# Optimization experiments

Hardware: AMD Instinct MI355X
Metric: run time of the kernel (lower is better)

## Reference

```python
import jax, jax.numpy as jnp
import numpy as np

N = 100000
INPLANES = 256
WIDTH = 104          # floor(256 * 26 / 64)
SCALE = 4
NUMS = SCALE - 1     # 3 branch convs
K = 27               # 3^3 kernel offsets for 3D kernel_size=3
EPS = 1e-5


def setup_inputs() -> dict:
    key = jax.random.key(0)
    ks = jax.random.split(key, 12)
    x_feat = jax.random.normal(ks[0], (N, INPLANES), dtype=jnp.float32)
    # neighbor map: index N means "no neighbor" (padded zero row)
    nbr_idx = jax.random.randint(ks[1], (N, K), 0, N + 1)
    ws = WIDTH * SCALE
    W1 = jax.random.normal(ks[2], (INPLANES, ws), dtype=jnp.float32) * (1.0 / np.sqrt(INPLANES))
    g1 = jnp.ones((ws,), jnp.float32)
    b1 = jnp.zeros((ws,), jnp.float32)
    Wc = jax.random.normal(ks[3], (NUMS, K, WIDTH, WIDTH), dtype=jnp.float32) * (1.0 / np.sqrt(K * WIDTH))
    gc = jnp.ones((NUMS, WIDTH), jnp.float32)
    bc = jnp.zeros((NUMS, WIDTH), jnp.float32)
    W3 = jax.random.normal(ks[4], (ws, INPLANES), dtype=jnp.float32) * (1.0 / np.sqrt(ws))
    g3 = jnp.ones((INPLANES,), jnp.float32)
    b3 = jnp.zeros((INPLANES,), jnp.float32)
    return {"x_feat": x_feat, "nbr_idx": nbr_idx, "W1": W1, "g1": g1, "b1": b1,
            "Wc": Wc, "gc": gc, "bc": bc, "W3": W3, "g3": g3, "b3": b3}


def _bn(x, g, b):
    # training-mode batch norm over the point dimension
    m = jnp.mean(x, axis=0)
    v = jnp.var(x, axis=0)
    return (x - m) * jax.lax.rsqrt(v + EPS) * g + b


def _sparse_conv(feat, nbr_idx, Wk):
    # gather-GEMM-scatter sparse conv: out[n] = sum_k feat[nbr[n,k]] @ Wk[k]
    # index == N hits the appended zero row (missing neighbor)
    fp = jnp.concatenate([feat, jnp.zeros((1, feat.shape[1]), feat.dtype)], axis=0)
    out = jnp.zeros((feat.shape[0], Wk.shape[2]), feat.dtype)
    for k in range(Wk.shape[0]):  # fixed small set of 27 kernel offsets
        out = out + fp[nbr_idx[:, k]] @ Wk[k]
    return out


def reference(x_feat, nbr_idx, W1, g1, b1, Wc, gc, bc, W3, g3, b3):
    out = jax.nn.relu(_bn(x_feat @ W1, g1, b1))          # [N, width*scale]
    spx = [out[:, i * WIDTH:(i + 1) * WIDTH] for i in range(SCALE)]
    parts = []
    sp = None
    for i in range(NUMS):
        # stype='normal', same coord map -> features_at_coordinates is identity
        sp_in = spx[i] if i == 0 else sp + spx[i]
        sp = jax.nn.relu(_bn(_sparse_conv(sp_in, nbr_idx, Wc[i]), gc[i], bc[i]))
        parts.append(sp)
    parts.append(spx[SCALE - 1])                          # scale != 1, normal
    cat = jnp.concatenate(parts, axis=1)                  # [N, width*scale]
    out = _bn(cat @ W3, g3, b3) + x_feat                  # residual (no downsample)
    return jax.nn.relu(out)
```

## Files before the change

### kernel.cpp

```cpp
#include <hip/hip_runtime.h>

#define NPTS 100000
#define INC 256
#define WID 104
#define WSC 416
#define KOFF 27
#define EPSV 1e-5f

typedef unsigned short u16;
typedef float f32x4 __attribute__((ext_vector_type(4)));
typedef short s16x8 __attribute__((ext_vector_type(8)));

__device__ __forceinline__ u16 f2bf(float f) {
  unsigned u = __builtin_bit_cast(unsigned, f);
  u += 0x7FFFu + ((u >> 16) & 1u);
  return (u16)(u >> 16);
}
__device__ __forceinline__ float bf2f(u16 h) {
  unsigned u = ((unsigned)h) << 16;
  return __builtin_bit_cast(float, u);
}
__device__ __forceinline__ void mfma16(f32x4& d, s16x8 a, s16x8 b) {
  asm("v_mfma_f32_16x16x32_bf16 %0, %1, %2, %0" : "+v"(d) : "v"(a), "v"(b));
}
__device__ __forceinline__ void rawbar() {
  __builtin_amdgcn_s_barrier();
  __builtin_amdgcn_sched_barrier(0);
}

#define ST1_OFF 0
#define STC0_OFF 7488
#define STC1_OFF 9360
#define STC2_OFF 11232
#define ST3_OFF 13104
#define ST_TOTAL 17712

__global__ __launch_bounds__(256) void k_prep_w1w3(const float* __restrict__ w1,
    const float* __restrict__ w3, u16* __restrict__ w1t, u16* __restrict__ w3t) {
  int i = blockIdx.x * 256 + threadIdx.x;
  if (i < 416 * 256) {
    int n = i >> 8, k = i & 255;
    w1t[i] = f2bf(w1[(size_t)k * WSC + n]);
  } else if (i < 2 * 416 * 256) {
    int o = i - 416 * 256;
    int n = o / WSC, k = o - n * WSC;
    w3t[o] = f2bf(w3[(size_t)k * INC + n]);
  }
}

__global__ __launch_bounds__(256) void k_prep_wc(const float* __restrict__ wc,
                                                 u16* __restrict__ wct) {
  __shared__ float w[WID * WID];
  int b = blockIdx.x, t = threadIdx.x;
  const float* s = wc + (size_t)b * WID * WID;
  for (int i = t; i < WID * WID; i += 256) w[i] = s[i];
  __syncthreads();
  u16* d = wct + (size_t)b * 112 * WID;
  for (int o = t; o < 112 * WID; o += 256) {
    int n = o / WID, kin = o - n * WID;
    d[o] = f2bf((n < WID) ? w[kin * WID + n] : 0.f);
  }
}

__global__ void k_init(float* __restrict__ st, u16* __restrict__ spxrow) {
  int i = blockIdx.x * 256 + threadIdx.x;
  if (i < ST_TOTAL) st[i] = 0.f;
  else if (i < ST_TOTAL + 104) spxrow[i - ST_TOTAL] = 0;
}

__global__ __launch_bounds__(256) void k_xbf(const float* __restrict__ x,
                                             u16* __restrict__ xb) {
  const int total = NPTS * INC / 8;
  for (int i = blockIdx.x * 256 + threadIdx.x; i < total; i += gridDim.x * 256) {
    const f32x4* s = (const f32x4*)(x + (size_t)i * 8);
    f32x4 v0 = s[0], v1 = s[1];
    s16x8 h;
#pragma unroll
    for (int j = 0; j < 4; ++j) { h[j] = (short)f2bf(v0[j]); h[4 + j] = (short)f2bf(v1[j]); }
    *(s16x8*)(xb + (size_t)i * 8) = h;
  }
}

__global__ __launch_bounds__(256) void k_gemm1(const u16* __restrict__ xb,
    const u16* __restrict__ w1t, u16* __restrict__ y1, float* __restrict__ stats) {
  __shared__ char Al[128 * 128];
  __shared__ char Bl[112 * 128];
  const int t = threadIdx.x, rowbase = blockIdx.x * 128, cb = blockIdx.y;
  const int lane = t & 63, wv = t >> 6, lr = lane & 15, lg = lane >> 4;
  const f32x4 fz = {0.f, 0.f, 0.f, 0.f};
  const s16x8 hz = {0, 0, 0, 0, 0, 0, 0, 0};
  f32x4 acc[2][7];
#pragma unroll
  for (int i = 0; i < 2; ++i)
#pragma unroll
    for (int j = 0; j < 7; ++j) acc[i][j] = fz;
  s16x8 pa[4], pb[4];

  auto issue = [&](int st) {
#pragma unroll
    for (int it = 0; it < 4; ++it) {
      int task = t + it * 256, r = task >> 3, c = task & 7, gr = rowbase + r;
      pa[it] = hz;
      if (gr < NPTS) pa[it] = *(const s16x8*)(xb + (size_t)gr * INC + st * 64 + c * 8);
      pb[it] = hz;
      if (task < 832)
        pb[it] = *(const s16x8*)(w1t + (size_t)(cb * WID + r) * INC + st * 64 + c * 8);
    }
  };
  auto writeT = [&]() {
#pragma unroll
    for (int it = 0; it < 4; ++it) {
      int task = t + it * 256, r = task >> 3, c = task & 7;
      *(s16x8*)(Al + ((r * 128 + c * 16) ^ ((r & 7) << 4))) = pa[it];
      if (task < 896) *(s16x8*)(Bl + ((r * 128 + c * 16) ^ ((r & 7) << 4))) = pb[it];
    }
  };
  auto compute = [&]() {
#pragma unroll
    for (int kc = 0; kc < 2; ++kc) {
      int co = kc * 64 + lg * 16;
      s16x8 a[2], b[7];
#pragma unroll
      for (int mt = 0; mt < 2; ++mt) {
        int r = wv * 32 + mt * 16 + lr;
        a[mt] = *(const s16x8*)(Al + ((r * 128 + co) ^ ((r & 7) << 4)));
      }
#pragma unroll
      for (int ct = 0; ct < 7; ++ct) {
        int r = ct * 16 + lr;
        b[ct] = *(const s16x8*)(Bl + ((r * 128 + co) ^ ((r & 7) << 4)));
      }
#pragma unroll
      for (int mt = 0; mt < 2; ++mt)
#pragma unroll
        for (int ct = 0; ct < 7; ++ct) mfma16(acc[mt][ct], a[mt], b[ct]);
    }
  };

  issue(0);
  for (int st = 0; st < 4; ++st) {
    writeT();
    __syncthreads();
    if (st < 3) issue(st + 1);
    compute();
    if (st < 3) rawbar();
  }
  __syncthreads();
  float* S = (float*)Al;
#pragma unroll
  for (int ct = 0; ct < 7; ++ct) {
    float s = 0.f, q = 0.f;
#pragma unroll
    for (int mt = 0; mt < 2; ++mt)
#pragma unroll
      for (int j = 0; j < 4; ++j) { float v = acc[mt][ct][j]; s += v; q += v * v; }
    s += __shfl_xor(s, 16); s += __shfl_xor(s, 32);
    q += __shfl_xor(q, 16); q += __shfl_xor(q, 32);
    if (lane < 16) {
      S[wv * 224 + ct * 16 + lane] = s;
      S[wv * 224 + 112 + ct * 16 + lane] = q;
    }
  }
  __syncthreads();
  if (t < 224) {
    float v = S[t] + S[224 + t] + S[448 + t] + S[672 + t];
    int cl = (t < 112) ? t : t - 112;
    if (cl < WID) {
      float* base = stats + (blockIdx.x & 7) * 832;
      atomicAdd(base + ((t < 112) ? 0 : WSC) + cb * WID + cl, v);
    }
  }
  __syncthreads();
#pragma unroll
  for (int mt = 0; mt < 2; ++mt)
#pragma unroll
    for (int ct = 0; ct < 7; ++ct)
#pragma unroll
      for (int j = 0; j < 4; ++j) {
        int r = rowbase + wv * 32 + mt * 16 + lg * 4 + j;
        int cl = ct * 16 + lr;
        if (r < NPTS && cl < WID)
          y1[(size_t)r * WSC + cb * WID + cl] = f2bf(acc[mt][ct][j]);
      }
}

__global__ __launch_bounds__(256) void k_conv(const u16* __restrict__ src,
    const int* __restrict__ nbr, const u16* __restrict__ wct,
    u16* __restrict__ z, float* __restrict__ stats) {
  __shared__ char Al[128 * 208];
  __shared__ char Bl[112 * 208];
  const int t = threadIdx.x, rowbase = blockIdx.x * 128;
  const int lane = t & 63, wv = t >> 6, lr = lane & 15, lg = lane >> 4;
  const f32x4 fz = {0.f, 0.f, 0.f, 0.f};
  const s16x8 hz = {0, 0, 0, 0, 0, 0, 0, 0};
  f32x4 acc[2][7];
#pragma unroll
  for (int i = 0; i < 2; ++i)
#pragma unroll
    for (int j = 0; j < 7; ++j) acc[i][j] = fz;
  s16x8 pa[8], pb[6];
  int pidx[8];

  auto idxIssue = [&](int kk) {
#pragma unroll
    for (int it = 0; it < 8; ++it) {
      int r = (t + it * 256) >> 4, gr = rowbase + r;
      pidx[it] = (gr < NPTS) ? nbr[gr * KOFF + kk] : NPTS;
    }
  };
  auto gatherIssue = [&]() {
#pragma unroll
    for (int it = 0; it < 8; ++it) {
      int c = (t + it * 256) & 15;
      pa[it] = hz;
      if (c < 13)
        pa[it] = *(const s16x8*)(src + (size_t)pidx[it] * WID + c * 8);
    }
  };
  auto loadB = [&](int k) {
#pragma unroll
    for (int it = 0; it < 6; ++it) {
      int task = t + it * 256;
      if (task < 1456) {
        int r = task / 13, c = task - 13 * r;
        pb[it] = *(const s16x8*)(wct + ((size_t)k * 112 + r) * WID + c * 8);
      }
    }
  };
  auto writeA = [&]() {
#pragma unroll
    for (int it = 0; it < 8; ++it) {
      int task = t + it * 256, r = task >> 4, c = task & 15;
      if (c < 13) *(s16x8*)(Al + r * 208 + c * 16) = pa[it];
    }
  };
  auto writeB = [&]() {
#pragma unroll
    for (int it = 0; it < 6; ++it) {
      int task = t + it * 256;
      if (task < 1456) {
        int r = task / 13, c = task - 13 * r;
        *(s16x8*)(Bl + r * 208 + c * 16) = pb[it];
      }
    }
  };
  auto compute = [&]() {
#pragma unroll
    for (int kc = 0; kc < 3; ++kc) {
      int co = kc * 64 + lg * 16;
      s16x8 a[2], b[7];
#pragma unroll
      for (int mt = 0; mt < 2; ++mt)
        a[mt] = *(const s16x8*)(Al + (wv * 32 + mt * 16 + lr) * 208 + co);
#pragma unroll
      for (int ct = 0; ct < 7; ++ct)
        b[ct] = *(const s16x8*)(Bl + (ct * 16 + lr) * 208 + co);
#pragma unroll
      for (int mt = 0; mt < 2; ++mt)
#pragma unroll
        for (int ct = 0; ct < 7; ++ct) mfma16(acc[mt][ct], a[mt], b[ct]);
    }
    {
      s16x8 a[2], b[7];
#pragma unroll
      for (int mt = 0; mt < 2; ++mt)
        a[mt] = (lg == 0) ? *(const s16x8*)(Al + (wv * 32 + mt * 16 + lr) * 208 + 192) : hz;
#pragma unroll
      for (int ct = 0; ct < 7; ++ct)
        b[ct] = (lg == 0) ? *(const s16x8*)(Bl + (ct * 16 + lr) * 208 + 192) : hz;
#pragma unroll
      for (int mt = 0; mt < 2; ++mt)
#pragma unroll
        for (int ct = 0; ct < 7; ++ct) mfma16(acc[mt][ct], a[mt], b[ct]);
    }
  };

  idxIssue(0);
  gatherIssue();
  loadB(0);
  idxIssue(1);
  for (int k = 0; k < KOFF; ++k) {
    writeA();
    writeB();
    __syncthreads();
    if (k < KOFF - 1) {
      gatherIssue();
      loadB(k + 1);
      if (k < KOFF - 2) idxIssue(k + 2);
    }
    compute();
    if (k < KOFF - 1) rawbar();
  }
  __syncthreads();
  float* S = (float*)Al;
#pragma unroll
  for (int ct = 0; ct < 7; ++ct) {
    float s = 0.f, q = 0.f;
#pragma unroll
    for (int mt = 0; mt < 2; ++mt)
#pragma unroll
      for (int j = 0; j < 4; ++j) { float v = acc[mt][ct][j]; s += v; q += v * v; }
    s += __shfl_xor(s, 16); s += __shfl_xor(s, 32);
    q += __shfl_xor(q, 16); q += __shfl_xor(q, 32);
    if (lane < 16) {
      S[wv * 224 + ct * 16 + lane] = s;
      S[wv * 224 + 112 + ct * 16 + lane] = q;
    }
  }
  __syncthreads();
  if (t < 224) {
    float v = S[t] + S[224 + t] + S[448 + t] + S[672 + t];
    int cl = (t < 112) ? t : t - 112;
    if (cl < WID) {
      float* base = stats + (blockIdx.x & 7) * 208;
      atomicAdd(base + ((t < 112) ? 0 : WID) + cl, v);
    }
  }
  __syncthreads();
#pragma unroll
  for (int mt = 0; mt < 2; ++mt)
#pragma unroll
    for (int ct = 0; ct < 7; ++ct)
#pragma unroll
      for (int j = 0; j < 4; ++j) {
        int r = rowbase + wv * 32 + mt * 16 + lg * 4 + j;
        int cl = ct * 16 + lr;
        if (r < NPTS && cl < WID)
          z[(size_t)r * WID + cl] = f2bf(acc[mt][ct][j]);
      }
}

__global__ __launch_bounds__(256) void k_gemm3(const u16* __restrict__ z0,
    const u16* __restrict__ z1, const u16* __restrict__ z2, const u16* __restrict__ y1,
    const u16* __restrict__ w3t, const float* __restrict__ ST, float* __restrict__ out,
    float* __restrict__ st3) {
  __shared__ char Al[128 * 128];
  __shared__ char Bl[128 * 128];
  __shared__ float sscl[416], ssft[416];
  const int t = threadIdx.x, rowbase = blockIdx.x * 128, cb = blockIdx.y;
  const int lane = t & 63, wv = t >> 6, lr = lane & 15, lg = lane >> 4;
  const int wr = wv >> 1, wc = wv & 1;
  const f32x4 fz = {0.f, 0.f, 0.f, 0.f};
  const s16x8 hz = {0, 0, 0, 0, 0, 0, 0, 0};
  for (int i = t; i < 416; i += 256) {
    float sc, sh;
    if (i < 312) {
      int p = i / 104, c = i - p * 104;
      const float* S = ST + STC0_OFF + p * 1872;
      sc = S[1664 + c]; sh = S[1768 + c];
    } else { sc = ST[6656 + i]; sh = ST[7072 + i]; }
    sscl[i] = sc; ssft[i] = sh;
  }
  f32x4 acc[4][4];
#pragma unroll
  for (int i = 0; i < 4; ++i)
#pragma unroll
    for (int j = 0; j < 4; ++j) acc[i][j] = fz;
  s16x8 pa[4], pb[4];

  auto issue = [&](int st) {
#pragma unroll
    for (int it = 0; it < 4; ++it) {
      int task = t + it * 256, r = task >> 3, c = task & 7;
      int gr = rowbase + r, gc = st * 8 + c;
      pa[it] = hz;
      if (gr < NPTS && gc < 52) {
        int p = gc / 13, cc8 = (gc - p * 13) * 8;
        const u16* s = (p == 0) ? z0 + (size_t)gr * WID + cc8
                     : (p == 1) ? z1 + (size_t)gr * WID + cc8
                     : (p == 2) ? z2 + (size_t)gr * WID + cc8
                                : y1 + (size_t)gr * WSC + 312 + cc8;
        pa[it] = *(const s16x8*)s;
      }
      int gk = st * 64 + c * 8;
      pb[it] = hz;
      if (gk < WSC) pb[it] = *(const s16x8*)(w3t + (size_t)(cb * 128 + r) * WSC + gk);
    }
  };
  auto writeT = [&](int st) {
#pragma unroll
    for (int it = 0; it < 4; ++it) {
      int task = t + it * 256, r = task >> 3, c = task & 7;
      int gr = rowbase + r, gc = st * 8 + c;
      s16x8 h = hz;
      if (gr < NPTS && gc < 52) {
        int p = gc / 13;
        int colb = p * WID + (gc - p * 13) * 8;
#pragma unroll
        for (int j = 0; j < 8; ++j) {
          float f = fmaxf(bf2f((u16)pa[it][j]) * sscl[colb + j] + ssft[colb + j], 0.f);
          h[j] = (short)f2bf(f);
        }
      }
      *(s16x8*)(Al + ((r * 128 + c * 16) ^ ((r & 7) << 4))) = h;
      *(s16x8*)(Bl + ((r * 128 + c * 16) ^ ((r & 7) << 4))) = pb[it];
    }
  };
  auto compute = [&]() {
#pragma unroll
    for (int kc = 0; kc < 2; ++kc) {
      int co = kc * 64 + lg * 16;
      s16x8 a[4], b[4];
#pragma unroll
      for (int mt = 0; mt < 4; ++mt) {
        int r = wr * 64 + mt * 16 + lr;
        a[mt] = *(const s16x8*)(Al + ((r * 128 + co) ^ ((r & 7) << 4)));
      }
#pragma unroll
      for (int ct = 0; ct < 4; ++ct) {
        int r = wc * 64 + ct * 16 + lr;
        b[ct] = *(const s16x8*)(Bl + ((r * 128 + co) ^ ((r & 7) << 4)));
      }
#pragma unroll
      for (int mt = 0; mt < 4; ++mt)
#pragma unroll
        for (int ct = 0; ct < 4; ++ct) mfma16(acc[mt][ct], a[mt], b[ct]);
    }
  };

  issue(0);
  __syncthreads();
  for (int st = 0; st < 7; ++st) {
    writeT(st);
    __syncthreads();
    if (st < 6) issue(st + 1);
    compute();
    if (st < 6) rawbar();
  }
  __syncthreads();
  float* S = (float*)Al;
#pragma unroll
  for (int ct = 0; ct < 4; ++ct) {
    float s = 0.f, q = 0.f;
#pragma unroll
    for (int mt = 0; mt < 4; ++mt)
#pragma unroll
      for (int j = 0; j < 4; ++j) { float v = acc[mt][ct][j]; s += v; q += v * v; }
    s += __shfl_xor(s, 16); s += __shfl_xor(s, 32);
    q += __shfl_xor(q, 16); q += __shfl_xor(q, 32);
    if (lane < 16) {
      S[wv * 128 + ct * 16 + lane] = s;
      S[wv * 128 + 64 + ct * 16 + lane] = q;
    }
  }
  __syncthreads();
  {
    float* base = st3 + (blockIdx.x & 7) * 512;
    if (t < 64) atomicAdd(base + cb * 128 + t, S[t] + S[256 + t]);
    else if (t < 128) atomicAdd(base + INC + cb * 128 + (t - 64), S[64 + t - 64] + S[320 + t - 64]);
    else if (t < 192) atomicAdd(base + cb * 128 + 64 + (t - 128), S[128 + t - 128] + S[384 + t - 128]);
    else atomicAdd(base + INC + cb * 128 + 64 + (t - 192), S[192 + t - 192] + S[448 + t - 192]);
  }
#pragma unroll
  for (int mt = 0; mt < 4; ++mt)
#pragma unroll
    for (int ct = 0; ct < 4; ++ct)
#pragma unroll
      for (int j = 0; j < 4; ++j) {
        int r = rowbase + wr * 64 + mt * 16 + lg * 4 + j;
        int col = cb * 128 + wc * 64 + ct * 16 + lr;
        if (r < NPTS) out[(size_t)r * INC + col] = acc[mt][ct][j];
      }
}

__global__ __launch_bounds__(512) void k_finstats(float* st, const float* __restrict__ g,
                                                  const float* __restrict__ b, int C) {
  int c = threadIdx.x;
  if (c < C) {
    float s = 0.f, q = 0.f;
#pragma unroll
    for (int bk = 0; bk < 8; ++bk) { s += st[bk * 2 * C + c]; q += st[bk * 2 * C + C + c]; }
    float m = s * (1.f / NPTS);
    float var = q * (1.f / NPTS) - m * m;
    float rs = rsqrtf(var + EPSV);
    float sc = rs * g[c];
    st[16 * C + c] = sc;
    st[17 * C + c] = b[c] - m * sc;
  }
}

template <int HASZ>
__global__ __launch_bounds__(256) void k_mix(const u16* __restrict__ y1, int yoff,
    const float* __restrict__ scl1, const float* __restrict__ sft1,
    const u16* __restrict__ z, const float* __restrict__ sclc, const float* __restrict__ sftc,
    u16* __restrict__ spx) {
  const int total = NPTS * 13;
  for (int i = blockIdx.x * 256 + threadIdx.x; i < total; i += gridDim.x * 256) {
    int r = i / 13, cc = i - r * 13;
    s16x8 y = *(const s16x8*)(y1 + (size_t)r * WSC + yoff + cc * 8);
    s16x8 zv;
    if (HASZ) zv = *(const s16x8*)(z + (size_t)r * WID + cc * 8);
    s16x8 o;
#pragma unroll
    for (int j = 0; j < 8; ++j) {
      int c = cc * 8 + j;
      float f = fmaxf(bf2f((u16)y[j]) * scl1[c] + sft1[c], 0.f);
      if (HASZ) f += fmaxf(bf2f((u16)zv[j]) * sclc[c] + sftc[c], 0.f);
      o[j] = (short)f2bf(f);
    }
    *(s16x8*)(spx + (size_t)r * WID + cc * 8) = o;
  }
}

__global__ __launch_bounds__(256) void k_final(float* __restrict__ y,
    const float* __restrict__ scale, const float* __restrict__ shift,
    const float* __restrict__ x) {
  const int total = NPTS * 64;
  for (int i = blockIdx.x * 256 + threadIdx.x; i < total; i += gridDim.x * 256) {
    int r = i >> 6, cc = i & 63;
    f32x4 v = *(f32x4*)(y + (size_t)r * INC + cc * 4);
    f32x4 xf = *(const f32x4*)(x + (size_t)r * INC + cc * 4);
#pragma unroll
    for (int j = 0; j < 4; ++j) {
      int c = cc * 4 + j;
      v[j] = fmaxf(v[j] * scale[c] + shift[c] + xf[j], 0.f);
    }
    *(f32x4*)(y + (size_t)r * INC + cc * 4) = v;
  }
}

extern "C" void kernel_launch(void* const* d_in, const int* in_sizes, int n_in,
                              void* d_out, int out_size, void* d_ws, size_t ws_size,
                              hipStream_t stream) {
  const float* x  = (const float*)d_in[0];
  const int* nbr  = (const int*)d_in[1];
  const float* W1 = (const float*)d_in[2];
  const float* g1 = (const float*)d_in[3];
  const float* b1 = (const float*)d_in[4];
  const float* Wc = (const float*)d_in[5];
  const float* gc = (const float*)d_in[6];
  const float* bc = (const float*)d_in[7];
  const float* W3 = (const float*)d_in[8];
  const float* g3 = (const float*)d_in[9];
  const float* b3 = (const float*)d_in[10];
  float* out = (float*)d_out;

  char* ws = (char*)d_ws;
  size_t off = 0;
  auto alloc = [&](size_t n) {
    char* p = ws + off;
    off += (n + 255) & ~(size_t)255;
    return p;
  };
  u16* W1T = (u16*)alloc(416 * 256 * 2);
  u16* W3T = (u16*)alloc(256 * 416 * 2);
  u16* WCT = (u16*)alloc((size_t)3 * 27 * 112 * 104 * 2);
  u16* XB  = (u16*)alloc((size_t)NPTS * INC * 2);
  u16* Y1  = (u16*)alloc((size_t)NPTS * WSC * 2);
  u16* Z0  = (u16*)alloc((size_t)NPTS * WID * 2);
  u16* Z1  = (u16*)alloc((size_t)NPTS * WID * 2);
  u16* Z2  = (u16*)alloc((size_t)NPTS * WID * 2);
  u16* SPX = (u16*)alloc((size_t)(NPTS + 1) * WID * 2);
  float* ST = (float*)alloc(ST_TOTAL * 4);
  float* ST1  = ST + ST1_OFF;
  float* STC0 = ST + STC0_OFF;
  float* STC1 = ST + STC1_OFF;
  float* STC2 = ST + STC2_OFF;
  float* ST3  = ST + ST3_OFF;

  k_prep_w1w3<<<832, 256, 0, stream>>>(W1, W3, W1T, W3T);
  k_prep_wc<<<81, 256, 0, stream>>>(Wc, WCT);
  k_init<<<70, 256, 0, stream>>>(ST, SPX + (size_t)NPTS * WID);
  k_xbf<<<2048, 256, 0, stream>>>(x, XB);

  k_gemm1<<<dim3(782, 4), 256, 0, stream>>>(XB, W1T, Y1, ST1);
  k_finstats<<<1, 512, 0, stream>>>(ST1, g1, b1, WSC);

  const size_t WCL = (size_t)27 * 112 * WID;
  k_mix<0><<<2048, 256, 0, stream>>>(Y1, 0, ST1 + 6656, ST1 + 7072, nullptr, nullptr, nullptr, SPX);
  k_conv<<<782, 256, 0, stream>>>(SPX, nbr, WCT, Z0, STC0);
  k_finstats<<<1, 512, 0, stream>>>(STC0, gc, bc, WID);
  k_mix<1><<<2048, 256, 0, stream>>>(Y1, 104, ST1 + 6656 + 104, ST1 + 7072 + 104,
                                     Z0, STC0 + 1664, STC0 + 1768, SPX);
  k_conv<<<782, 256, 0, stream>>>(SPX, nbr, WCT + WCL, Z1, STC1);
  k_finstats<<<1, 512, 0, stream>>>(STC1, gc + 104, bc + 104, WID);
  k_mix<1><<<2048, 256, 0, stream>>>(Y1, 208, ST1 + 6656 + 208, ST1 + 7072 + 208,
                                     Z1, STC1 + 1664, STC1 + 1768, SPX);
  k_conv<<<782, 256, 0, stream>>>(SPX, nbr, WCT + 2 * WCL, Z2, STC2);
  k_finstats<<<1, 512, 0, stream>>>(STC2, gc + 208, bc + 208, WID);

  k_gemm3<<<dim3(782, 2), 256, 0, stream>>>(Z0, Z1, Z2, Y1, W3T, ST, out, ST3);
  k_finstats<<<1, 512, 0, stream>>>(ST3, g3, b3, INC);
  k_final<<<2048, 256, 0, stream>>>(out, ST3 + 4096, ST3 + 4352, x);
}
```

Measured before the change: 751.8 us.

## Gather conv operands directly into MFMA fragments, bypassing LDS staging

The sparse conv kernel no longer stages gathered neighbor rows and weights through shared memory. Each lane loads its A fragment straight from a 128-padded SPX buffer, and B fragments come from weights pre-packed into MFMA lane order, with software double-buffering across K-chunks. This removes LDS writes/reads and the per-offset barriers and allows three blocks per CU. The cost is more redundant global and L2 traffic, since each wave loads all weight fragments itself, plus a padded activation buffer with a zero-initialised tail.

After: 1.302 ms. +73.1%, slower.

```diff
diff --git a/kernel.cpp b/kernel.cpp
--- a/kernel.cpp
+++ b/kernel.cpp
@@ -34,6 +34,8 @@
 #define STC2_OFF 11232
 #define ST3_OFF 13104
 #define ST_TOTAL 17712
+
+#define SPAD 128
 
 __global__ __launch_bounds__(256) void k_prep_w1w3(const float* __restrict__ w1,
     const float* __restrict__ w3, u16* __restrict__ w1t, u16* __restrict__ w3t) {
@@ -49,23 +51,39 @@
 }
 
 __global__ __launch_bounds__(256) void k_prep_wc(const float* __restrict__ wc,
-                                                 u16* __restrict__ wct) {
+                                                 u16* __restrict__ wcf) {
   __shared__ float w[WID * WID];
-  int b = blockIdx.x, t = threadIdx.x;
-  const float* s = wc + (size_t)b * WID * WID;
+  int blk = blockIdx.x, t = threadIdx.x;
+  const float* s = wc + (size_t)blk * WID * WID;
   for (int i = t; i < WID * WID; i += 256) w[i] = s[i];
   __syncthreads();
-  u16* d = wct + (size_t)b * 112 * WID;
-  for (int o = t; o < 112 * WID; o += 256) {
-    int n = o / WID, kin = o - n * WID;
-    d[o] = f2bf((n < WID) ? w[kin * WID + n] : 0.f);
-  }
-}
-
-__global__ void k_init(float* __restrict__ st, u16* __restrict__ spxrow) {
+  u16* d = wcf + (size_t)blk * 28 * 512;
+  for (int task = t; task < 28 * 64; task += 256) {
+    int frag = task >> 6, l = task & 63;
+    int ct = frag >> 2, kc = frag & 3;
+    int n = ct * 16 + (l & 15);
+    int kb = kc * 32 + (l >> 4) * 8;
+    s16x8 h;
+#pragma unroll
+    for (int j = 0; j < 8; ++j) {
+      int kin = kb + j;
+      float v = (kin < WID && n < WID) ? w[kin * WID + n] : 0.f;
+      h[j] = (short)f2bf(v);
+    }
+    *(s16x8*)(d + (size_t)task * 8) = h;
+  }
+}
+
+__global__ void k_init(float* __restrict__ st, u16* __restrict__ spxp) {
+  const s16x8 hz = {0, 0, 0, 0, 0, 0, 0, 0};
   int i = blockIdx.x * 256 + threadIdx.x;
   if (i < ST_TOTAL) st[i] = 0.f;
-  else if (i < ST_TOTAL + 104) spxrow[i - ST_TOTAL] = 0;
+  for (int task = i; task < (NPTS + 1) * 3; task += gridDim.x * 256) {
+    int r = task / 3, c = task - 3 * r;
+    *(s16x8*)(spxp + (size_t)r * SPAD + (13 + c) * 8) = hz;
+  }
+  if (blockIdx.x == 0 && threadIdx.x < 13)
+    *(s16x8*)(spxp + (size_t)NPTS * SPAD + threadIdx.x * 8) = hz;
 }
 
 __global__ __launch_bounds__(256) void k_xbf(const float* __restrict__ x,
@@ -184,115 +202,70 @@
       }
 }
 
-__global__ __launch_bounds__(256) void k_conv(const u16* __restrict__ src,
-    const int* __restrict__ nbr, const u16* __restrict__ wct,
+__global__ __launch_bounds__(256, 3) void k_conv(const u16* __restrict__ src,
+    const int* __restrict__ nbr, const u16* __restrict__ wcf,
     u16* __restrict__ z, float* __restrict__ stats) {
-  __shared__ char Al[128 * 208];
-  __shared__ char Bl[112 * 208];
+  __shared__ float S[896];
   const int t = threadIdx.x, rowbase = blockIdx.x * 128;
   const int lane = t & 63, wv = t >> 6, lr = lane & 15, lg = lane >> 4;
+  const int ch = lg * 8;
   const f32x4 fz = {0.f, 0.f, 0.f, 0.f};
-  const s16x8 hz = {0, 0, 0, 0, 0, 0, 0, 0};
   f32x4 acc[2][7];
 #pragma unroll
   for (int i = 0; i < 2; ++i)
 #pragma unroll
     for (int j = 0; j < 7; ++j) acc[i][j] = fz;
-  s16x8 pa[8], pb[6];
-  int pidx[8];
-
-  auto idxIssue = [&](int kk) {
-#pragma unroll
-    for (int it = 0; it < 8; ++it) {
-      int r = (t + it * 256) >> 4, gr = rowbase + r;
-      pidx[it] = (gr < NPTS) ? nbr[gr * KOFF + kk] : NPTS;
-    }
-  };
-  auto gatherIssue = [&]() {
-#pragma unroll
-    for (int it = 0; it < 8; ++it) {
-      int c = (t + it * 256) & 15;
-      pa[it] = hz;
-      if (c < 13)
-        pa[it] = *(const s16x8*)(src + (size_t)pidx[it] * WID + c * 8);
-    }
-  };
-  auto loadB = [&](int k) {
-#pragma unroll
-    for (int it = 0; it < 6; ++it) {
-      int task = t + it * 256;
-      if (task < 1456) {
-        int r = task / 13, c = task - 13 * r;
-        pb[it] = *(const s16x8*)(wct + ((size_t)k * 112 + r) * WID + c * 8);
-      }
-    }
-  };
-  auto writeA = [&]() {
-#pragma unroll
-    for (int it = 0; it < 8; ++it) {
-      int task = t + it * 256, r = task >> 4, c = task & 15;
-      if (c < 13) *(s16x8*)(Al + r * 208 + c * 16) = pa[it];
-    }
-  };
-  auto writeB = [&]() {
-#pragma unroll
-    for (int it = 0; it < 6; ++it) {
-      int task = t + it * 256;
-      if (task < 1456) {
-        int r = task / 13, c = task - 13 * r;
-        *(s16x8*)(Bl + r * 208 + c * 16) = pb[it];
-      }
-    }
-  };
-  auto compute = [&]() {
-#pragma unroll
-    for (int kc = 0; kc < 3; ++kc) {
-      int co = kc * 64 + lg * 16;
-      s16x8 a[2], b[7];
-#pragma unroll
-      for (int mt = 0; mt < 2; ++mt)
-        a[mt] = *(const s16x8*)(Al + (wv * 32 + mt * 16 + lr) * 208 + co);
-#pragma unroll
-      for (int ct = 0; ct < 7; ++ct)
-        b[ct] = *(const s16x8*)(Bl + (ct * 16 + lr) * 208 + co);
-#pragma unroll
-      for (int mt = 0; mt < 2; ++mt)
-#pragma unroll
-        for (int ct = 0; ct < 7; ++ct) mfma16(acc[mt][ct], a[mt], b[ct]);
-    }
-    {
-      s16x8 a[2], b[7];
-#pragma unroll
-      for (int mt = 0; mt < 2; ++mt)
-        a[mt] = (lg == 0) ? *(const s16x8*)(Al + (wv * 32 + mt * 16 + lr) * 208 + 192) : hz;
-#pragma unroll
-      for (int ct = 0; ct < 7; ++ct)
-        b[ct] = (lg == 0) ? *(const s16x8*)(Bl + (ct * 16 + lr) * 208 + 192) : hz;
-#pragma unroll
-      for (int mt = 0; mt < 2; ++mt)
-#pragma unroll
-        for (int ct = 0; ct < 7; ++ct) mfma16(acc[mt][ct], a[mt], b[ct]);
-    }
-  };
-
-  idxIssue(0);
-  gatherIssue();
-  loadB(0);
-  idxIssue(1);
+
+  const int rm0 = rowbase + wv * 32 + lr;
+  const int rm1 = rm0 + 16;
+  const bool ok0 = rm0 < NPTS, ok1 = rm1 < NPTS;
+  const int* np0 = nbr + (size_t)(ok0 ? rm0 : 0) * KOFF;
+  const int* np1 = nbr + (size_t)(ok1 ? rm1 : 0) * KOFF;
+  const u16* bp = wcf + (size_t)lane * 8;
+
+  s16x8 aC0, aC1, aN0, aN1;
+  s16x8 bf[7];
+  int ic0, ic1, in0, in1;
+
+  auto GA = [&](int i0, int i1, int kc, s16x8& d0, s16x8& d1) {
+    d0 = *(const s16x8*)(src + (size_t)i0 * SPAD + kc * 32 + ch);
+    d1 = *(const s16x8*)(src + (size_t)i1 * SPAD + kc * 32 + ch);
+  };
+  auto LB = [&](int k, int kc) {
+#pragma unroll
+    for (int ct = 0; ct < 7; ++ct)
+      bf[ct] = *(const s16x8*)(bp + (size_t)(k * 28 + ct * 4 + kc) * 512);
+  };
+  auto MM = [&](s16x8& a0, s16x8& a1) {
+#pragma unroll
+    for (int ct = 0; ct < 7; ++ct) {
+      mfma16(acc[0][ct], a0, bf[ct]);
+      mfma16(acc[1][ct], a1, bf[ct]);
+    }
+  };
+
+  ic0 = ok0 ? np0[0] : NPTS;
+  ic1 = ok1 ? np1[0] : NPTS;
+  GA(ic0, ic1, 0, aC0, aC1);
+  in0 = ok0 ? np0[1] : NPTS;
+  in1 = ok1 ? np1[1] : NPTS;
+
   for (int k = 0; k < KOFF; ++k) {
-    writeA();
-    writeB();
-    __syncthreads();
-    if (k < KOFF - 1) {
-      gatherIssue();
-      loadB(k + 1);
-      if (k < KOFF - 2) idxIssue(k + 2);
-    }
-    compute();
-    if (k < KOFF - 1) rawbar();
-  }
-  __syncthreads();
-  float* S = (float*)Al;
+    LB(k, 0); GA(ic0, ic1, 1, aN0, aN1); MM(aC0, aC1);
+    LB(k, 1); GA(ic0, ic1, 2, aC0, aC1); MM(aN0, aN1);
+    LB(k, 2); GA(ic0, ic1, 3, aN0, aN1); MM(aC0, aC1);
+    LB(k, 3);
+    if (k < KOFF - 1) GA(in0, in1, 0, aC0, aC1);
+    MM(aN0, aN1);
+    int t0 = NPTS, t1 = NPTS;
+    if (k < KOFF - 2) {
+      t0 = ok0 ? np0[k + 2] : NPTS;
+      t1 = ok1 ? np1[k + 2] : NPTS;
+    }
+    ic0 = in0; ic1 = in1; in0 = t0; in1 = t1;
+  }
+
+  __syncthreads();
 #pragma unroll
   for (int ct = 0; ct < 7; ++ct) {
     float s = 0.f, q = 0.f;
@@ -316,7 +289,6 @@
       atomicAdd(base + ((t < 112) ? 0 : WID) + cl, v);
     }
   }
-  __syncthreads();
 #pragma unroll
   for (int mt = 0; mt < 2; ++mt)
 #pragma unroll
@@ -498,7 +470,7 @@
       if (HASZ) f += fmaxf(bf2f((u16)zv[j]) * sclc[c] + sftc[c], 0.f);
       o[j] = (short)f2bf(f);
     }
-    *(s16x8*)(spx + (size_t)r * WID + cc * 8) = o;
+    *(s16x8*)(spx + (size_t)r * SPAD + cc * 8) = o;
   }
 }
 
@@ -544,13 +516,13 @@
   };
   u16* W1T = (u16*)alloc(416 * 256 * 2);
   u16* W3T = (u16*)alloc(256 * 416 * 2);
-  u16* WCT = (u16*)alloc((size_t)3 * 27 * 112 * 104 * 2);
+  u16* WCF = (u16*)alloc((size_t)3 * 27 * 28 * 512 * 2);
   u16* XB  = (u16*)alloc((size_t)NPTS * INC * 2);
   u16* Y1  = (u16*)alloc((size_t)NPTS * WSC * 2);
   u16* Z0  = (u16*)alloc((size_t)NPTS * WID * 2);
   u16* Z1  = (u16*)alloc((size_t)NPTS * WID * 2);
   u16* Z2  = (u16*)alloc((size_t)NPTS * WID * 2);
-  u16* SPX = (u16*)alloc((size_t)(NPTS + 1) * WID * 2);
+  u16* SPX = (u16*)alloc((size_t)(NPTS + 1) * SPAD * 2);
   float* ST = (float*)alloc(ST_TOTAL * 4);
   float* ST1  = ST + ST1_OFF;
   float* STC0 = ST + STC0_OFF;
@@ -559,24 +531,24 @@
   float* ST3  = ST + ST3_OFF;
 
   k_prep_w1w3<<<832, 256, 0, stream>>>(W1, W3, W1T, W3T);
-  k_prep_wc<<<81, 256, 0, stream>>>(Wc, WCT);
-  k_init<<<70, 256, 0, stream>>>(ST, SPX + (size_t)NPTS * WID);
+  k_prep_wc<<<81, 256, 0, stream>>>(Wc, WCF);
+  k_init<<<256, 256, 0, stream>>>(ST, SPX);
   k_xbf<<<2048, 256, 0, stream>>>(x, XB);
 
   k_gemm1<<<dim3(782, 4), 256, 0, stream>>>(XB, W1T, Y1, ST1);
   k_finstats<<<1, 512, 0, stream>>>(ST1, g1, b1, WSC);
 
-  const size_t WCL = (size_t)27 * 112 * WID;
+  const size_t WCL = (size_t)27 * 28 * 512;
   k_mix<0><<<2048, 256, 0, stream>>>(Y1, 0, ST1 + 6656, ST1 + 7072, nullptr, nullptr, nullptr, SPX);
-  k_conv<<<782, 256, 0, stream>>>(SPX, nbr, WCT, Z0, STC0);
+  k_conv<<<782, 256, 0, stream>>>(SPX, nbr, WCF, Z0, STC0);
   k_finstats<<<1, 512, 0, stream>>>(STC0, gc, bc, WID);
   k_mix<1><<<2048, 256, 0, stream>>>(Y1, 104, ST1 + 6656 + 104, ST1 + 7072 + 104,
                                      Z0, STC0 + 1664, STC0 + 1768, SPX);
-  k_conv<<<782, 256, 0, stream>>>(SPX, nbr, WCT + WCL, Z1, STC1);
+  k_conv<<<782, 256, 0, stream>>>(SPX, nbr, WCF + WCL, Z1, STC1);
   k_finstats<<<1, 512, 0, stream>>>(STC1, gc + 104, bc + 104, WID);
   k_mix<1><<<2048, 256, 0, stream>>>(Y1, 208, ST1 + 6656 + 208, ST1 + 7072 + 208,
                                      Z1, STC1 + 1664, STC1 + 1768, SPX);
-  k_conv<<<782, 256, 0, stream>>>(SPX, nbr, WCT + 2 * WCL, Z2, STC2);
+  k_conv<<<782, 256, 0, stream>>>(SPX, nbr, WCF + 2 * WCL, Z2, STC2);
   k_finstats<<<1, 512, 0, stream>>>(STC2, gc + 208, bc + 208, WID);
 
   k_gemm3<<<dim3(782, 2), 256, 0, stream>>>(Z0, Z1, Z2, Y1, W3T, ST, out, ST3);
```
